# Optimization experiments

Measured on AMD Instinct MI355X. Metric: run time of the kernel, lower is better.

Reference implementation:

```python
import jax, jax.numpy as jnp
import numpy as np
from jax import lax

BOS = 0
B, T, U = 8, 256, 64
IN, ENC_H, DEC_H, P, J, V = 80, 512, 512, 512, 512, 1024


def lstm_layer(x, Wih, Whh, b):
    """PyTorch-style LSTM layer. x: [B,T,I]; Wih: [4H,I]; Whh: [4H,H]; b: [4H]."""
    Bn = x.shape[0]
    H = Whh.shape[1]
    xp = jnp.einsum('bti,gi->btg', x, Wih) + b  # precompute input projections [B,T,4H]
    h0 = jnp.zeros((Bn, H), x.dtype)

    def step(carry, xt):
        h, c = carry
        g = xt + h @ Whh.T
        i, f, gg, o = jnp.split(g, 4, axis=-1)
        c = jax.nn.sigmoid(f) * c + jax.nn.sigmoid(i) * jnp.tanh(gg)
        h = jax.nn.sigmoid(o) * jnp.tanh(c)
        return (h, c), h

    _, hs = lax.scan(step, (h0, h0), xp.transpose(1, 0, 2))
    return hs.transpose(1, 0, 2)  # [B,T,H]


def setup_inputs() -> dict:
    key = jax.random.key(0)
    ks = jax.random.split(key, 20)
    s = 0.04  # ~1/sqrt(H) init scale
    inp = {
        'xs': jax.random.normal(ks[0], (B, T, IN), jnp.float32),
        'ys': jax.random.randint(ks[1], (B, U), 0, V),
        # encoder LSTM layer 0 / 1
        'enc_Wih0': jax.random.normal(ks[2], (4 * ENC_H, IN), jnp.float32) * s,
        'enc_Whh0': jax.random.normal(ks[3], (4 * ENC_H, ENC_H), jnp.float32) * s,
        'enc_b0': jnp.zeros((4 * ENC_H,), jnp.float32),
        'enc_Wih1': jax.random.normal(ks[4], (4 * ENC_H, ENC_H), jnp.float32) * s,
        'enc_Whh1': jax.random.normal(ks[5], (4 * ENC_H, ENC_H), jnp.float32) * s,
        'enc_b1': jnp.zeros((4 * ENC_H,), jnp.float32),
        'enc_projW': jax.random.normal(ks[6], (P, ENC_H), jnp.float32) * s,
        'enc_projb': jnp.zeros((P,), jnp.float32),
        # decoder
        'embed': jax.random.normal(ks[7], (V, DEC_H), jnp.float32) * s,
        'dec_Wih': jax.random.normal(ks[8], (4 * DEC_H, DEC_H), jnp.float32) * s,
        'dec_Whh': jax.random.normal(ks[9], (4 * DEC_H, DEC_H), jnp.float32) * s,
        'dec_b': jnp.zeros((4 * DEC_H,), jnp.float32),
        'dec_projW': jax.random.normal(ks[10], (P, DEC_H), jnp.float32) * s,
        'dec_projb': jnp.zeros((P,), jnp.float32),
        # joint MLP: Linear(2P -> J), Tanh, Linear(J -> V)
        'jW1': jax.random.normal(ks[11], (J, 2 * P), jnp.float32) * s,
        'jb1': jnp.zeros((J,), jnp.float32),
        'jW2': jax.random.normal(ks[12], (V, J), jnp.float32) * s,
        'jb2': jnp.zeros((V,), jnp.float32),
    }
    return inp


def reference(xs, ys, enc_Wih0, enc_Whh0, enc_b0, enc_Wih1, enc_Whh1, enc_b1,
              enc_projW, enc_projb, embed, dec_Wih, dec_Whh, dec_b,
              dec_projW, dec_projb, jW1, jb1, jW2, jb2):
    # Encoder: 2-layer LSTM + projection
    h = lstm_layer(xs, enc_Wih0, enc_Whh0, enc_b0)
    h = lstm_layer(h, enc_Wih1, enc_Whh1, enc_b1)
    h_enc = h @ enc_projW.T + enc_projb  # [B,T,P]

    # Decoder: BOS pad, embed, 1-layer LSTM + projection
    ys_p = jnp.pad(ys, ((0, 0), (1, 0)), constant_values=BOS)  # [B,U+1]
    e = embed[ys_p]
    hd = lstm_layer(e, dec_Wih, dec_Whh, dec_b)
    h_dec = hd @ dec_projW.T + dec_projb  # [B,U+1,P]

    # Joint: cat([h_enc,h_dec]) @ W1.T == h_enc @ W1[:,:P].T + h_dec @ W1[:,P:].T
    pre_enc = jnp.einsum('btp,jp->btj', h_enc, jW1[:, :P])
    pre_dec = jnp.einsum('bup,jp->buj', h_dec, jW1[:, P:])
    z = jnp.tanh(pre_enc[:, :, None, :] + pre_dec[:, None, :, :] + jb1)  # [B,T,U+1,J]
    logits = jnp.einsum('btuj,vj->btuv', z, jW2) + jb2  # [B,T,U+1,V]
    return logits
```

## Files before the change

### kernel.cpp

```cpp
#include <hip/hip_runtime.h>


typedef _Float16 f16;
typedef _Float16 f16x8 __attribute__((ext_vector_type(8)));
typedef float f32x4 __attribute__((ext_vector_type(4)));
using u32 = unsigned int;

#define BB   8
#define TT   256
#define UU1  65
#define HH   512
#define G4   2048
#define PP   512
#define JJ   512
#define VV   1024
#define SENT 0xFFFFFFFFu

#define LOADX(p)     __hip_atomic_load((p), __ATOMIC_RELAXED, __HIP_MEMORY_SCOPE_AGENT)
#define STOREX(p, v) __hip_atomic_store((p), (v), __ATOMIC_RELAXED, __HIP_MEMORY_SCOPE_AGENT)

static __device__ __forceinline__ u32 packf16(float a, float b) {
  f16 ha = (f16)a, hb = (f16)b;
  unsigned short ua = __builtin_bit_cast(unsigned short, ha);
  unsigned short ub = __builtin_bit_cast(unsigned short, hb);
  return (u32)ua | ((u32)ub << 16);
}
static __device__ __forceinline__ float sigm(float x) {
  x = fminf(30.f, fmaxf(-30.f, x));
  return __builtin_amdgcn_rcpf(1.f + __expf(-x));
}
static __device__ __forceinline__ float ftanh(float x) {
  x = fminf(15.f, fmaxf(-15.f, x));
  float t = __expf(2.f * x);
  return (t - 1.f) * __builtin_amdgcn_rcpf(t + 1.f);
}

__global__ void k_init(u32* __restrict__ p, int n, int z1, int z2) {
  int i = blockIdx.x * 256 + threadIdx.x;
  if (i >= n) return;
  bool z = (i < 2048) | ((u32)(i - z1) < 2048u) | ((u32)(i - z2) < 2048u);
  p[i] = z ? 0u : SENT;
}

struct CastSeg { const float* s; f16* d; int n4; };
struct CastArgs { CastSeg seg[10]; };
__global__ void k_cast_all(CastArgs a, int total4) {
  int i = blockIdx.x * 256 + threadIdx.x;
  if (i >= total4) return;
  int k = 0, off = i;
  while (off >= a.seg[k].n4) { off -= a.seg[k].n4; ++k; }
  const float4 v = *(const float4*)(a.seg[k].s + (size_t)off * 4);
  uint2 p; p.x = packf16(v.x, v.y); p.y = packf16(v.z, v.w);
  *(uint2*)(a.seg[k].d + (size_t)off * 4) = p;
}

__global__ void k_embed(const int* __restrict__ ys, const float* __restrict__ emb,
                        float* __restrict__ e) {
  int row = blockIdx.x;
  int b = row / UU1, u = row % UU1;
  int idx = (u == 0) ? 0 : ys[b * (UU1 - 1) + (u - 1)];
  const float4* s = (const float4*)(emb + (size_t)idx * HH);
  float4* d = (float4*)(e + (size_t)row * HH);
  d[threadIdx.x] = s[threadIdx.x];
}

__global__ __launch_bounds__(256) void k_gemm(
    const float* __restrict__ A, const f16* __restrict__ B,
    const float* __restrict__ bias, float* __restrict__ C,
    int M, int N, int K, int lda, int ldb) {
  __shared__ f16 As[128][72];
  __shared__ f16 Bs[128][72];
  int tid = threadIdx.x;
  int mb = blockIdx.y * 128, nb = blockIdx.x * 128;
  int wave = tid >> 6, lane = tid & 63;
  int wm = wave >> 1, wn = wave & 1;
  int rowa = lane & 15, kg = lane >> 4;
  f32x4 acc[4][4] = {};
  for (int k0 = 0; k0 < K; k0 += 64) {
    for (int idx = tid; idx < 2048; idx += 256) {
      int r = idx >> 4, cq = idx & 15;
      int gm = mb + r, gk = k0 + cq * 4;
      float4 v = make_float4(0.f, 0.f, 0.f, 0.f);
      if (gm < M && gk + 3 < K) v = *(const float4*)(A + (size_t)gm * lda + gk);
      uint2 p; p.x = packf16(v.x, v.y); p.y = packf16(v.z, v.w);
      *(uint2*)&As[r][cq * 4] = p;
    }
    for (int idx = tid; idx < 1024; idx += 256) {
      int r = idx >> 3, c8 = idx & 7;
      int gn = nb + r, gk = k0 + c8 * 8;
      uint4 v = make_uint4(0u, 0u, 0u, 0u);
      if (gn < N && gk + 7 < K) v = *(const uint4*)(B + (size_t)gn * ldb + gk);
      *(uint4*)&Bs[r][c8 * 8] = v;
    }
    __syncthreads();
#pragma unroll
    for (int kf = 0; kf < 2; ++kf) {
      f16x8 af[4], bf[4];
#pragma unroll
      for (int mt = 0; mt < 4; ++mt)
        af[mt] = *(const f16x8*)&As[wm * 64 + mt * 16 + rowa][kf * 32 + kg * 8];
#pragma unroll
      for (int nt = 0; nt < 4; ++nt)
        bf[nt] = *(const f16x8*)&Bs[wn * 64 + nt * 16 + rowa][kf * 32 + kg * 8];
#pragma unroll
      for (int mt = 0; mt < 4; ++mt)
#pragma unroll
        for (int nt = 0; nt < 4; ++nt)
          acc[mt][nt] = __builtin_amdgcn_mfma_f32_16x16x32_f16(af[mt], bf[nt], acc[mt][nt], 0, 0, 0);
    }
    __syncthreads();
  }
#pragma unroll
  for (int nt = 0; nt < 4; ++nt) {
    int gn = nb + wn * 64 + nt * 16 + rowa;
    float bv = bias ? bias[gn] : 0.f;
#pragma unroll
    for (int mt = 0; mt < 4; ++mt)
#pragma unroll
      for (int r = 0; r < 4; ++r) {
        int gm = mb + wm * 64 + mt * 16 + kg * 4 + r;
        if (gm < M) C[(size_t)gm * N + gn] = acc[mt][nt][r] + bv;
      }
  }
}

template <int NW>
static __device__ __forceinline__ void poll_batch(const u32* const* p, u32* vv) {
#pragma unroll
  for (int k = 0; k < NW; ++k) vv[k] = LOADX(p[k]);
  int gd = 0;
  while (++gd < (1 << 18)) {
    bool any = false;
#pragma unroll
    for (int k = 0; k < NW; ++k) any = any | (vv[k] == SENT);
    if (!any) break;
    __builtin_amdgcn_s_sleep(4);
#pragma unroll
    for (int k = 0; k < NW; ++k)
      if (vv[k] == SENT) vv[k] = LOADX(p[k]);
  }
}
static __device__ __forceinline__ void guard_spin(const u32* gp) {
  u32 v = LOADX(gp);
  int gd = 0;
  while (v == SENT && ++gd < (1 << 18)) {
    __builtin_amdgcn_s_sleep(2);
    v = LOADX(gp);
  }
}

static __device__ __forceinline__ void lstm_16(
    int wg, const float* __restrict__ xp, const f16* __restrict__ Whh,
    u32* __restrict__ hseq,
    float* __restrict__ hs, int S) {
  extern __shared__ char smem[];
  f16 (*W)[520] = (f16(*)[520])smem;
  f16 (*H)[520] = (f16(*)[520])(smem + 133120);
  float (*gat)[8][36] = (float(*)[8][36])(smem + 133120 + 8320);
  const int tid = threadIdx.x;
  const int u0 = wg * 32;
  const int wave = tid >> 6, lane = tid & 63;
  const int rowa = lane & 15, kg = lane >> 4;
  const int b = lane >> 3, ju = lane & 7;
  const int uglob = u0 + wave * 8 + ju;

  for (int idx = tid; idx < 128 * 64; idx += 256) {
    int r = idx >> 6, ck = idx & 63;
    int w = r >> 5, g = (r >> 3) & 3, u = r & 7;
    uint4 v = *(const uint4*)(Whh + ((size_t)(g * 512 + u0 + w * 8 + u)) * 512 + ck * 8);
    *(uint4*)&W[r][ck * 8] = v;
  }
  __syncthreads();

  float c = 0.f;
  for (int t = 0; t < S; ++t) {
    const u32* hb = hseq + (size_t)t * 2048;
    if (tid < 16) guard_spin(hb + tid * 16);
    __syncthreads();

    size_t xpo = ((size_t)b * S + t) * (size_t)G4 + uglob;
    float xi = xp[xpo], xf = xp[xpo + 512], xg = xp[xpo + 1024], xo = xp[xpo + 1536];

    const u32* ptr[8];
    u32 vv[8];
#pragma unroll
    for (int k = 0; k < 8; ++k) ptr[k] = hb + ((tid + k * 256) >> 8) * 256 + ((tid + k * 256) & 255);
    poll_batch<8>(ptr, vv);
#pragma unroll
    for (int k = 0; k < 8; ++k) {
      int idx = tid + k * 256;
      ((u32*)H)[(idx >> 8) * 260 + (idx & 255)] = vv[k];
    }
    __syncthreads();

    f32x4 acc0 = {0.f, 0.f, 0.f, 0.f}, acc1 = {0.f, 0.f, 0.f, 0.f};
#pragma unroll
    for (int kf = 0; kf < 16; ++kf) {
      f16x8 af = {};
      if (rowa < 8) af = *(const f16x8*)&H[rowa][kf * 32 + kg * 8];
      f16x8 b0 = *(const f16x8*)&W[wave * 32 + rowa][kf * 32 + kg * 8];
      f16x8 b1 = *(const f16x8*)&W[wave * 32 + 16 + rowa][kf * 32 + kg * 8];
      acc0 = __builtin_amdgcn_mfma_f32_16x16x32_f16(af, b0, acc0, 0, 0, 0);
      acc1 = __builtin_amdgcn_mfma_f32_16x16x32_f16(af, b1, acc1, 0, 0, 0);
    }
    if (kg < 2) {
#pragma unroll
      for (int r = 0; r < 4; ++r) {
        gat[wave][kg * 4 + r][rowa] = acc0[r];
        gat[wave][kg * 4 + r][16 + rowa] = acc1[r];
      }
    }
    float gi = gat[wave][b][ju] + xi;
    float gf = gat[wave][b][8 + ju] + xf;
    float gg = gat[wave][b][16 + ju] + xg;
    float go = gat[wave][b][24 + ju] + xo;
    c = sigm(gf) * c + sigm(gi) * ftanh(gg);
    float h = sigm(go) * ftanh(c);

    float hn = __shfl_down(h, 1);
    if ((ju & 1) == 0)
      STOREX(hseq + (size_t)(t + 1) * 2048 + ((b * 512 + uglob) >> 1), packf16(h, hn));
    if (hs) hs[((size_t)b * S + t) * HH + uglob] = h;
  }
}

static __device__ __forceinline__ void lstm_l1(
    int wg, const float* __restrict__ gb, const f16* __restrict__ Wih,
    const f16* __restrict__ Whh, const u32* __restrict__ hin,
    u32* __restrict__ hseq, float* __restrict__ hs, int S) {
  extern __shared__ char smem[];
  f16 (*W)[1032] = (f16(*)[1032])smem;
  f16 (*H)[1032] = (f16(*)[1032])(smem + 132096);
  float (*gat)[8][20] = (float(*)[8][20])(smem + 132096 + 16512);
  const int tid = threadIdx.x;
  const int u0 = wg * 16;
  const int wave = tid >> 6, lane = tid & 63;
  const int rowa = lane & 15, kg = lane >> 4;
  const int b = lane >> 2, ju = lane & 3;
  const int uglob = u0 + wave * 4 + ju;

  for (int idx = tid; idx < 64 * 64; idx += 256) {
    int r = idx >> 6, ck = idx & 63;
    int w = r >> 4, g = (r >> 2) & 3, u = r & 3;
    size_t grow = (size_t)(g * 512 + u0 + w * 4 + u) * 512;
    *(uint4*)&W[r][ck * 8]       = *(const uint4*)(Whh + grow + ck * 8);
    *(uint4*)&W[r][512 + ck * 8] = *(const uint4*)(Wih + grow + ck * 8);
  }
  float gbi = 0.f, gbf = 0.f, gbg = 0.f, gbo = 0.f;
  if (lane < 32) {
    gbi = gb[uglob]; gbf = gb[512 + uglob];
    gbg = gb[1024 + uglob]; gbo = gb[1536 + uglob];
  }
  __syncthreads();

  float c = 0.f;
  for (int t = 0; t < S; ++t) {
    const u32* hbS = hseq + (size_t)t * 2048;
    const u32* hbU = hin + (size_t)(t + 1) * 2048;
    if (tid < 32)       guard_spin(hbS + tid * 8);
    else if (tid < 48)  guard_spin(hbU + (tid - 32) * 16);
    __syncthreads();
    const u32* ptr[16];
    u32 vv[16];
#pragma unroll
    for (int k = 0; k < 8; ++k) {
      int idx = tid + k * 256;
      int r = idx >> 8, cu = idx & 255;
      ptr[k] = hbS + r * 256 + cu;
      ptr[k + 8] = hbU + r * 256 + cu;
    }
    poll_batch<16>(ptr, vv);
#pragma unroll
    for (int k = 0; k < 8; ++k) {
      int idx = tid + k * 256;
      int r = idx >> 8, cu = idx & 255;
      ((u32*)H)[r * 516 + cu] = vv[k];
      ((u32*)H)[r * 516 + 256 + cu] = vv[k + 8];
    }
    __syncthreads();

    f32x4 accA = {0.f, 0.f, 0.f, 0.f}, accB = {0.f, 0.f, 0.f, 0.f};
#pragma unroll
    for (int kf = 0; kf < 16; ++kf) {
      f16x8 afA = {}, afB = {};
      if (rowa < 8) {
        afA = *(const f16x8*)&H[rowa][kf * 32 + kg * 8];
        afB = *(const f16x8*)&H[rowa][(kf + 16) * 32 + kg * 8];
      }
      f16x8 bfA = *(const f16x8*)&W[wave * 16 + rowa][kf * 32 + kg * 8];
      f16x8 bfB = *(const f16x8*)&W[wave * 16 + rowa][(kf + 16) * 32 + kg * 8];
      accA = __builtin_amdgcn_mfma_f32_16x16x32_f16(afA, bfA, accA, 0, 0, 0);
      accB = __builtin_amdgcn_mfma_f32_16x16x32_f16(afB, bfB, accB, 0, 0, 0);
    }
    if (kg < 2) {
#pragma unroll
      for (int r = 0; r < 4; ++r) gat[wave][kg * 4 + r][rowa] = accA[r] + accB[r];
    }
    if (lane < 32) {
      float gi = gat[wave][b][ju]      + gbi;
      float gf = gat[wave][b][4 + ju]  + gbf;
      float gg = gat[wave][b][8 + ju]  + gbg;
      float go = gat[wave][b][12 + ju] + gbo;
      c = sigm(gf) * c + sigm(gi) * ftanh(gg);
      float h = sigm(go) * ftanh(c);
      float hn = __shfl_down(h, 1);
      if ((ju & 1) == 0)
        STOREX(hseq + (size_t)(t + 1) * 2048 + (b * 256 + (uglob >> 1)), packf16(h, hn));
      hs[((size_t)b * S + t) * HH + uglob] = h;
    }
  }
}

__global__ __launch_bounds__(256, 1) void k_lstm3(
    const float* xp0, const f16* Whh0, u32* hseq0,
    const float* b1, const f16* Wih1, const f16* Whh1, u32* hseq1, float* h1s,
    const float* xpd, const f16* Whhd, u32* hseqD, float* hds) {
  int g = blockIdx.x;
  if (g < 16)      lstm_16(g, xp0, Whh0, hseq0, nullptr, TT);
  else if (g < 48) lstm_l1(g - 16, b1, Wih1, Whh1, hseq0, hseq1, h1s, TT);
  else             lstm_16(g - 48, xpd, Whhd, hseqD, hds, UU1);
}

__global__ __launch_bounds__(512) void k_joint(
    const float* __restrict__ pre_enc,
    const float* __restrict__ pre_dec,
    const f16* __restrict__ jW2,
    const float* __restrict__ jb2,
    float* __restrict__ out) {
  extern __shared__ char smem[];
  f16 (*Z)[520] = (f16(*)[520])smem;
  int tid = threadIdx.x;
  int m0 = blockIdx.x * 64;
  {
    int r = tid >> 3, q = tid & 7;
    int m = m0 + r;
    int bb = m / (TT * UU1);
    int rem = m % (TT * UU1);
    int t = rem / UU1, u = rem % UU1;
    const float* pe = pre_enc + ((size_t)bb * TT + t) * JJ + q * 64;
    const float* pd = pre_dec + ((size_t)bb * UU1 + u) * JJ + q * 64;
    for (int i = 0; i < 64; i += 8) {
      float4 e0 = *(const float4*)(pe + i);
      float4 e1 = *(const float4*)(pe + i + 4);
      float4 d0 = *(const float4*)(pd + i);
      float4 d1 = *(const float4*)(pd + i + 4);
      float z0 = ftanh(e0.x + d0.x), z1 = ftanh(e0.y + d0.y);
      float z2 = ftanh(e0.z + d0.z), z3 = ftanh(e0.w + d0.w);
      float z4 = ftanh(e1.x + d1.x), z5 = ftanh(e1.y + d1.y);
      float z6 = ftanh(e1.z + d1.z), z7 = ftanh(e1.w + d1.w);
      uint4 p; p.x = packf16(z0, z1); p.y = packf16(z2, z3);
      p.z = packf16(z4, z5); p.w = packf16(z6, z7);
      *(uint4*)&Z[r][q * 64 + i] = p;
    }
  }
  __syncthreads();
  int wave = tid >> 6, lane = tid & 63;
  int wm = wave >> 2, wn = wave & 3;
  int rowa = lane & 15, kg = lane >> 4;
  for (int ch = 0; ch < 4; ++ch) {
    f32x4 acc[4][2] = {};
    int nb = ch * 256 + wn * 64;
    for (int kf = 0; kf < 16; ++kf) {
      f16x8 af[4], bf[2];
#pragma unroll
      for (int nt = 0; nt < 4; ++nt)
        af[nt] = *(const f16x8*)(jW2 + (size_t)(nb + nt * 16 + rowa) * JJ + kf * 32 + kg * 8);
#pragma unroll
      for (int mt = 0; mt < 2; ++mt)
        bf[mt] = *(const f16x8*)&Z[wm * 32 + mt * 16 + rowa][kf * 32 + kg * 8];
#pragma unroll
      for (int nt = 0; nt < 4; ++nt)
#pragma unroll
        for (int mt = 0; mt < 2; ++mt)
          acc[nt][mt] = __builtin_amdgcn_mfma_f32_16x16x32_f16(af[nt], bf[mt], acc[nt][mt], 0, 0, 0);
    }
#pragma unroll
    for (int nt = 0; nt < 4; ++nt) {
      int v = nb + nt * 16 + kg * 4;
      float4 bv = *(const float4*)(jb2 + v);
#pragma unroll
      for (int mt = 0; mt < 2; ++mt) {
        int m = m0 + wm * 32 + mt * 16 + rowa;
        f32x4 st;
        st[0] = acc[nt][mt][0] + bv.x;
        st[1] = acc[nt][mt][1] + bv.y;
        st[2] = acc[nt][mt][2] + bv.z;
        st[3] = acc[nt][mt][3] + bv.w;
        __builtin_nontemporal_store(st, (f32x4*)(out + (size_t)m * VV + v));
      }
    }
  }
}

extern "C" void kernel_launch(void* const* d_in, const int* in_sizes, int n_in,
                              void* d_out, int out_size, void* d_ws, size_t ws_size,
                              hipStream_t stream) {
  const float* xs    = (const float*)d_in[0];
  const int*   ys    = (const int*)d_in[1];
  const float* Wih0  = (const float*)d_in[2];
  const float* Whh0  = (const float*)d_in[3];
  const float* b0    = (const float*)d_in[4];
  const float* Wih1  = (const float*)d_in[5];
  const float* Whh1  = (const float*)d_in[6];
  const float* b1    = (const float*)d_in[7];
  const float* encPW = (const float*)d_in[8];
  const float* encPb = (const float*)d_in[9];
  const float* embed = (const float*)d_in[10];
  const float* dWih  = (const float*)d_in[11];
  const float* dWhh  = (const float*)d_in[12];
  const float* db    = (const float*)d_in[13];
  const float* dPW   = (const float*)d_in[14];
  const float* dPb   = (const float*)d_in[15];
  const float* jW1   = (const float*)d_in[16];
  const float* jb1   = (const float*)d_in[17];
  const float* jW2   = (const float*)d_in[18];
  const float* jb2   = (const float*)d_in[19];
  float* out = (float*)d_out;

  char* base = (char*)d_ws;
  size_t off = 0;
  auto alc = [&](size_t bytes) -> char* {
    char* p = base + off;
    off = (off + bytes + 255) & ~(size_t)255;
    return p;
  };
  f16* Wih0h = (f16*)alc((size_t)2048 * 80 * 2);
  f16* Whh0h = (f16*)alc((size_t)2048 * 512 * 2);
  f16* Wih1h = (f16*)alc((size_t)2048 * 512 * 2);
  f16* Whh1h = (f16*)alc((size_t)2048 * 512 * 2);
  f16* dWihh = (f16*)alc((size_t)2048 * 512 * 2);
  f16* dWhhh = (f16*)alc((size_t)2048 * 512 * 2);
  f16* ePWh  = (f16*)alc((size_t)512 * 512 * 2);
  f16* dPWh  = (f16*)alc((size_t)512 * 512 * 2);
  f16* jW1h  = (f16*)alc((size_t)512 * 1024 * 2);
  f16* jW2h  = (f16*)alc((size_t)1024 * 512 * 2);
  float* e    = (float*)alc((size_t)520 * 512 * 4);
  float* xp0  = (float*)alc((size_t)2048 * 2048 * 4);
  float* xpd  = (float*)alc((size_t)520 * 2048 * 4);
  float* h1s  = (float*)alc((size_t)2048 * 512 * 4);
  float* hds  = (float*)alc((size_t)520 * 512 * 4);
  float* henc = (float*)alc((size_t)2048 * 512 * 4);
  float* hdec = (float*)alc((size_t)520 * 512 * 4);
  float* penc = (float*)alc((size_t)2048 * 512 * 4);
  float* pdec = (float*)alc((size_t)520 * 512 * 4);
  u32* hseq0 = (u32*)alc((size_t)(TT + 1) * 2048 * 4);
  u32* hseq1 = (u32*)alc((size_t)(TT + 1) * 2048 * 4);
  u32* hseqD = (u32*)alc((size_t)(UU1 + 1) * 2048 * 4);
  if (off > ws_size) return;

  {
    int n = (int)(((TT + 1) * 2 + (UU1 + 1)) * 2048);
    int z1 = (int)(hseq1 - hseq0), z2 = (int)(hseqD - hseq0);
    k_init<<<dim3((n + 255) / 256), dim3(256), 0, stream>>>(hseq0, n, z1, z2);
  }
  {
    CastArgs ca;
    auto seg = [&](int i, const float* s, f16* d, size_t n) {
      ca.seg[i].s = s; ca.seg[i].d = d; ca.seg[i].n4 = (int)(n / 4);
    };
    seg(0, Wih0, Wih0h, (size_t)2048 * 80);
    seg(1, Whh0, Whh0h, (size_t)2048 * 512);
    seg(2, Wih1, Wih1h, (size_t)2048 * 512);
    seg(3, Whh1, Whh1h, (size_t)2048 * 512);
    seg(4, dWih, dWihh, (size_t)2048 * 512);
    seg(5, dWhh, dWhhh, (size_t)2048 * 512);
    seg(6, encPW, ePWh, (size_t)512 * 512);
    seg(7, dPW, dPWh, (size_t)512 * 512);
    seg(8, jW1, jW1h, (size_t)512 * 1024);
    seg(9, jW2, jW2h, (size_t)1024 * 512);
    int total4 = 0;
    for (int i = 0; i < 10; ++i) total4 += ca.seg[i].n4;
    k_cast_all<<<dim3((total4 + 255) / 256), dim3(256), 0, stream>>>(ca, total4);
  }

  k_embed<<<dim3(520), dim3(128), 0, stream>>>(ys, embed, e);

  auto gemm = [&](const float* A, const f16* B, const float* bias, float* C,
                  int M, int N, int K, int lda, int ldb) {
    k_gemm<<<dim3(N / 128, (M + 127) / 128), dim3(256), 0, stream>>>(
        A, B, bias, C, M, N, K, lda, ldb);
  };

  gemm(xs, Wih0h, b0, xp0, 2048, 2048, 80, 80, 80);
  gemm(e, dWihh, db, xpd, 520, 2048, 512, 512, 512);

  k_lstm3<<<dim3(64), dim3(256), 151168, stream>>>(
      xp0, Whh0h, hseq0,
      b1, Wih1h, Whh1h, hseq1, h1s,
      xpd, dWhhh, hseqD, hds);

  gemm(h1s, ePWh, encPb, henc, 2048, 512, 512, 512, 512);
  gemm(henc, jW1h, nullptr, penc, 2048, 512, 512, 512, 1024);
  gemm(hds, dPWh, dPb, hdec, 520, 512, 512, 512, 512);
  gemm(hdec, jW1h + 512, jb1, pdec, 520, 512, 512, 512, 1024);

  k_joint<<<dim3(2080), dim3(512), 66560, stream>>>(penc, pdec, jW2h, jb2, out);
}
```

Before: 1.589 ms.

## Fold projection weights into joint W1, split LSTM recurrence wait, prefetch joint weights

Precomputes the products jW1_enc·encProjW and jW1_dec·decProjW, plus the folded biases, so that each side of the joint needs one GEMM instead of two chained ones. This removes four activation GEMMs and replaces them with two. In the layer-1 LSTM wavefront, the input-side half of the matvec now runs before the block waits on its own layer's previous hidden state, which overlaps part of the recurrence latency. The joint kernel double-buffers its jW2 fragment loads from global memory so the loads overlap the MFMAs. The folded weights are rounded to fp16 after an extra multiplication, which changes precision slightly.

```diff
diff --git a/kernel.cpp b/kernel.cpp
--- a/kernel.cpp
+++ b/kernel.cpp
@@ -62,6 +62,23 @@
   const float4* s = (const float4*)(emb + (size_t)idx * HH);
   float4* d = (float4*)(e + (size_t)row * HH);
   d[threadIdx.x] = s[threadIdx.x];
+}
+
+__global__ void k_biasdot(const float* __restrict__ jW1, const float* __restrict__ encPb,
+                          const float* __restrict__ dPb, const float* __restrict__ jb1,
+                          float* __restrict__ bce, float* __restrict__ bcd) {
+  int j = blockIdx.x * 256 + threadIdx.x;
+  if (j >= 512) return;
+  const float* rowE = jW1 + (size_t)j * 1024;
+  const float* rowD = rowE + 512;
+  float s1 = 0.f, s2 = 0.f;
+  for (int p = 0; p < 512; p += 4) {
+    float4 a = *(const float4*)(rowE + p), b = *(const float4*)(encPb + p);
+    s1 += a.x * b.x + a.y * b.y + a.z * b.z + a.w * b.w;
+    float4 c = *(const float4*)(rowD + p), d = *(const float4*)(dPb + p);
+    s2 += c.x * d.x + c.y * d.y + c.z * d.z + c.w * d.w;
+  }
+  bce[j] = s1; bcd[j] = s2 + jb1[j];
 }
 
 __global__ __launch_bounds__(256) void k_gemm(
@@ -124,6 +141,62 @@
   }
 }
 
+__global__ __launch_bounds__(256) void k_gemmT(
+    const float* __restrict__ A, int lda, const f16* __restrict__ B2,
+    f16* __restrict__ C16) {
+  __shared__ f16 As[128][72];
+  __shared__ f16 Bs[128][72];
+  int tid = threadIdx.x;
+  int mb = blockIdx.y * 128, nb = blockIdx.x * 128;
+  int wave = tid >> 6, lane = tid & 63;
+  int wm = wave >> 1, wn = wave & 1;
+  int rowa = lane & 15, kg = lane >> 4;
+  f32x4 acc[4][4] = {};
+  for (int k0 = 0; k0 < 512; k0 += 64) {
+    for (int idx = tid; idx < 2048; idx += 256) {
+      int r = idx >> 4, cq = idx & 15;
+      float4 v = *(const float4*)(A + (size_t)(mb + r) * lda + k0 + cq * 4);
+      uint2 p; p.x = packf16(v.x, v.y); p.y = packf16(v.z, v.w);
+      *(uint2*)&As[r][cq * 4] = p;
+    }
+    for (int idx = tid; idx < 1024; idx += 256) {
+      int r = idx >> 4, c8 = idx & 15;
+      uint4 v = *(const uint4*)(B2 + (size_t)(k0 + r) * 512 + nb + c8 * 8);
+      f16 tmp[8]; *(uint4*)tmp = v;
+#pragma unroll
+      for (int e = 0; e < 8; ++e) Bs[c8 * 8 + e][r] = tmp[e];
+    }
+    __syncthreads();
+#pragma unroll
+    for (int kf = 0; kf < 2; ++kf) {
+      f16x8 af[4], bf[4];
+#pragma unroll
+      for (int mt = 0; mt < 4; ++mt)
+        af[mt] = *(const f16x8*)&As[wm * 64 + mt * 16 + rowa][kf * 32 + kg * 8];
+#pragma unroll
+      for (int nt = 0; nt < 4; ++nt)
+        bf[nt] = *(const f16x8*)&Bs[wn * 64 + nt * 16 + rowa][kf * 32 + kg * 8];
+#pragma unroll
+      for (int mt = 0; mt < 4; ++mt)
+#pragma unroll
+        for (int nt = 0; nt < 4; ++nt)
+          acc[mt][nt] = __builtin_amdgcn_mfma_f32_16x16x32_f16(af[mt], bf[nt], acc[mt][nt], 0, 0, 0);
+    }
+    __syncthreads();
+  }
+#pragma unroll
+  for (int nt = 0; nt < 4; ++nt) {
+    int gn = nb + wn * 64 + nt * 16 + rowa;
+#pragma unroll
+    for (int mt = 0; mt < 4; ++mt)
+#pragma unroll
+      for (int r = 0; r < 4; ++r) {
+        int gm = mb + wm * 64 + mt * 16 + kg * 4 + r;
+        C16[(size_t)gm * 512 + gn] = (f16)acc[mt][nt][r];
+      }
+  }
+}
+
 template <int NW>
 static __device__ __forceinline__ void poll_batch(const u32* const* p, u32* vv) {
 #pragma unroll
@@ -257,38 +330,66 @@
   for (int t = 0; t < S; ++t) {
     const u32* hbS = hseq + (size_t)t * 2048;
     const u32* hbU = hin + (size_t)(t + 1) * 2048;
-    if (tid < 32)       guard_spin(hbS + tid * 8);
-    else if (tid < 48)  guard_spin(hbU + (tid - 32) * 16);
-    __syncthreads();
-    const u32* ptr[16];
-    u32 vv[16];
-#pragma unroll
-    for (int k = 0; k < 8; ++k) {
-      int idx = tid + k * 256;
-      int r = idx >> 8, cu = idx & 255;
-      ptr[k] = hbS + r * 256 + cu;
-      ptr[k + 8] = hbU + r * 256 + cu;
-    }
-    poll_batch<16>(ptr, vv);
-#pragma unroll
-    for (int k = 0; k < 8; ++k) {
-      int idx = tid + k * 256;
-      int r = idx >> 8, cu = idx & 255;
-      ((u32*)H)[r * 516 + cu] = vv[k];
-      ((u32*)H)[r * 516 + 256 + cu] = vv[k + 8];
-    }
-    __syncthreads();
-
+
+    if (tid < 16) guard_spin(hbU + tid * 16);
+    __syncthreads();
+    {
+      const u32* ptr[8];
+      u32 vv[8];
+#pragma unroll
+      for (int k = 0; k < 8; ++k) {
+        int idx = tid + k * 256;
+        ptr[k] = hbU + (idx >> 8) * 256 + (idx & 255);
+      }
+      poll_batch<8>(ptr, vv);
+#pragma unroll
+      for (int k = 0; k < 8; ++k) {
+        int idx = tid + k * 256;
+        ((u32*)H)[(idx >> 8) * 516 + 256 + (idx & 255)] = vv[k];
+      }
+    }
+    __syncthreads();
     f32x4 accA = {0.f, 0.f, 0.f, 0.f}, accB = {0.f, 0.f, 0.f, 0.f};
 #pragma unroll
-    for (int kf = 0; kf < 16; ++kf) {
+    for (int kf = 0; kf < 8; ++kf) {
+      f16x8 afA = {}, afB = {};
+      if (rowa < 8) {
+        afA = *(const f16x8*)&H[rowa][(16 + kf) * 32 + kg * 8];
+        afB = *(const f16x8*)&H[rowa][(24 + kf) * 32 + kg * 8];
+      }
+      f16x8 bfA = *(const f16x8*)&W[wave * 16 + rowa][(16 + kf) * 32 + kg * 8];
+      f16x8 bfB = *(const f16x8*)&W[wave * 16 + rowa][(24 + kf) * 32 + kg * 8];
+      accA = __builtin_amdgcn_mfma_f32_16x16x32_f16(afA, bfA, accA, 0, 0, 0);
+      accB = __builtin_amdgcn_mfma_f32_16x16x32_f16(afB, bfB, accB, 0, 0, 0);
+    }
+
+    if (tid < 32) guard_spin(hbS + tid * 8);
+    __syncthreads();
+    {
+      const u32* ptr[8];
+      u32 vv[8];
+#pragma unroll
+      for (int k = 0; k < 8; ++k) {
+        int idx = tid + k * 256;
+        ptr[k] = hbS + (idx >> 8) * 256 + (idx & 255);
+      }
+      poll_batch<8>(ptr, vv);
+#pragma unroll
+      for (int k = 0; k < 8; ++k) {
+        int idx = tid + k * 256;
+        ((u32*)H)[(idx >> 8) * 516 + (idx & 255)] = vv[k];
+      }
+    }
+    __syncthreads();
+#pragma unroll
+    for (int kf = 0; kf < 8; ++kf) {
       f16x8 afA = {}, afB = {};
       if (rowa < 8) {
         afA = *(const f16x8*)&H[rowa][kf * 32 + kg * 8];
-        afB = *(const f16x8*)&H[rowa][(kf + 16) * 32 + kg * 8];
+        afB = *(const f16x8*)&H[rowa][(8 + kf) * 32 + kg * 8];
       }
       f16x8 bfA = *(const f16x8*)&W[wave * 16 + rowa][kf * 32 + kg * 8];
-      f16x8 bfB = *(const f16x8*)&W[wave * 16 + rowa][(kf + 16) * 32 + kg * 8];
+      f16x8 bfB = *(const f16x8*)&W[wave * 16 + rowa][(8 + kf) * 32 + kg * 8];
       accA = __builtin_amdgcn_mfma_f32_16x16x32_f16(afA, bfA, accA, 0, 0, 0);
       accB = __builtin_amdgcn_mfma_f32_16x16x32_f16(afB, bfB, accB, 0, 0, 0);
     }
@@ -360,19 +461,40 @@
   for (int ch = 0; ch < 4; ++ch) {
     f32x4 acc[4][2] = {};
     int nb = ch * 256 + wn * 64;
-    for (int kf = 0; kf < 16; ++kf) {
-      f16x8 af[4], bf[2];
+    const f16* wb = jW2 + (size_t)(nb + rowa) * JJ + kg * 8;
+    f16x8 afe[4], afo[4];
+#pragma unroll
+    for (int nt = 0; nt < 4; ++nt)
+      afe[nt] = *(const f16x8*)(wb + (size_t)nt * 16 * JJ);
+#pragma unroll
+    for (int kp = 0; kp < 8; ++kp) {
+      const int kfe = kp * 2, kfo = kp * 2 + 1;
 #pragma unroll
       for (int nt = 0; nt < 4; ++nt)
-        af[nt] = *(const f16x8*)(jW2 + (size_t)(nb + nt * 16 + rowa) * JJ + kf * 32 + kg * 8);
-#pragma unroll
-      for (int mt = 0; mt < 2; ++mt)
-        bf[mt] = *(const f16x8*)&Z[wm * 32 + mt * 16 + rowa][kf * 32 + kg * 8];
-#pragma unroll
-      for (int nt = 0; nt < 4; ++nt)
-#pragma unroll
-        for (int mt = 0; mt < 2; ++mt)
-          acc[nt][mt] = __builtin_amdgcn_mfma_f32_16x16x32_f16(af[nt], bf[mt], acc[nt][mt], 0, 0, 0);
+        afo[nt] = *(const f16x8*)(wb + (size_t)nt * 16 * JJ + kfo * 32);
+      {
+        f16x8 bf0 = *(const f16x8*)&Z[wm * 32 + rowa][kfe * 32 + kg * 8];
+        f16x8 bf1 = *(const f16x8*)&Z[wm * 32 + 16 + rowa][kfe * 32 + kg * 8];
+#pragma unroll
+        for (int nt = 0; nt < 4; ++nt) {
+          acc[nt][0] = __builtin_amdgcn_mfma_f32_16x16x32_f16(afe[nt], bf0, acc[nt][0], 0, 0, 0);
+          acc[nt][1] = __builtin_amdgcn_mfma_f32_16x16x32_f16(afe[nt], bf1, acc[nt][1], 0, 0, 0);
+        }
+      }
+      if (kp < 7) {
+#pragma unroll
+        for (int nt = 0; nt < 4; ++nt)
+          afe[nt] = *(const f16x8*)(wb + (size_t)nt * 16 * JJ + (kfe + 2) * 32);
+      }
+      {
+        f16x8 bf0 = *(const f16x8*)&Z[wm * 32 + rowa][kfo * 32 + kg * 8];
+        f16x8 bf1 = *(const f16x8*)&Z[wm * 32 + 16 + rowa][kfo * 32 + kg * 8];
+#pragma unroll
+        for (int nt = 0; nt < 4; ++nt) {
+          acc[nt][0] = __builtin_amdgcn_mfma_f32_16x16x32_f16(afo[nt], bf0, acc[nt][0], 0, 0, 0);
+          acc[nt][1] = __builtin_amdgcn_mfma_f32_16x16x32_f16(afo[nt], bf1, acc[nt][1], 0, 0, 0);
+        }
+      }
     }
 #pragma unroll
     for (int nt = 0; nt < 4; ++nt) {
@@ -432,15 +554,16 @@
   f16* dWhhh = (f16*)alc((size_t)2048 * 512 * 2);
   f16* ePWh  = (f16*)alc((size_t)512 * 512 * 2);
   f16* dPWh  = (f16*)alc((size_t)512 * 512 * 2);
-  f16* jW1h  = (f16*)alc((size_t)512 * 1024 * 2);
   f16* jW2h  = (f16*)alc((size_t)1024 * 512 * 2);
+  f16* Wceh  = (f16*)alc((size_t)512 * 512 * 2);
+  f16* Wcdh  = (f16*)alc((size_t)512 * 512 * 2);
+  float* bce  = (float*)alc((size_t)512 * 4);
+  float* bcd  = (float*)alc((size_t)512 * 4);
   float* e    = (float*)alc((size_t)520 * 512 * 4);
   float* xp0  = (float*)alc((size_t)2048 * 2048 * 4);
   float* xpd  = (float*)alc((size_t)520 * 2048 * 4);
   float* h1s  = (float*)alc((size_t)2048 * 512 * 4);
   float* hds  = (float*)alc((size_t)520 * 512 * 4);
-  float* henc = (float*)alc((size_t)2048 * 512 * 4);
-  float* hdec = (float*)alc((size_t)520 * 512 * 4);
   float* penc = (float*)alc((size_t)2048 * 512 * 4);
   float* pdec = (float*)alc((size_t)520 * 512 * 4);
   u32* hseq0 = (u32*)alc((size_t)(TT + 1) * 2048 * 4);
@@ -454,7 +577,7 @@
     k_init<<<dim3((n + 255) / 256), dim3(256), 0, stream>>>(hseq0, n, z1, z2);
   }
   {
-    CastArgs ca;
+    CastArgs ca = {};
     auto seg = [&](int i, const float* s, f16* d, size_t n) {
       ca.seg[i].s = s; ca.seg[i].d = d; ca.seg[i].n4 = (int)(n / 4);
     };
@@ -466,12 +589,14 @@
     seg(5, dWhh, dWhhh, (size_t)2048 * 512);
     seg(6, encPW, ePWh, (size_t)512 * 512);
     seg(7, dPW, dPWh, (size_t)512 * 512);
-    seg(8, jW1, jW1h, (size_t)512 * 1024);
-    seg(9, jW2, jW2h, (size_t)1024 * 512);
+    seg(8, jW2, jW2h, (size_t)1024 * 512);
     int total4 = 0;
-    for (int i = 0; i < 10; ++i) total4 += ca.seg[i].n4;
+    for (int i = 0; i < 9; ++i) total4 += ca.seg[i].n4;
     k_cast_all<<<dim3((total4 + 255) / 256), dim3(256), 0, stream>>>(ca, total4);
   }
+  k_gemmT<<<dim3(4, 4), dim3(256), 0, stream>>>(jW1, 1024, ePWh, Wceh);
+  k_gemmT<<<dim3(4, 4), dim3(256), 0, stream>>>(jW1 + 512, 1024, dPWh, Wcdh);
+  k_biasdot<<<dim3(2), dim3(256), 0, stream>>>(jW1, encPb, dPb, jb1, bce, bcd);
 
   k_embed<<<dim3(520), dim3(128), 0, stream>>>(ys, embed, e);
 
@@ -489,10 +614,8 @@
       b1, Wih1h, Whh1h, hseq1, h1s,
       xpd, dWhhh, hseqD, hds);
 
-  gemm(h1s, ePWh, encPb, henc, 2048, 512, 512, 512, 512);
-  gemm(henc, jW1h, nullptr, penc, 2048, 512, 512, 512, 1024);
-  gemm(hds, dPWh, dPb, hdec, 520, 512, 512, 512, 512);
-  gemm(hdec, jW1h + 512, jb1, pdec, 520, 512, 512, 512, 1024);
+  gemm(h1s, Wceh, bce, penc, 2048, 512, 512, 512, 512);
+  gemm(hds, Wcdh, bcd, pdec, 520, 512, 512, 512, 512);
 
   k_joint<<<dim3(2080), dim3(512), 66560, stream>>>(penc, pdec, jW2h, jb2, out);
 }
```

After: 1.658 ms. 4.3% more time.
